# Performance work log

Measured on AMD Instinct MI355X. Metric: run time of the kernel, lower is better.

The kernel has to match this reference:

```python
import jax, jax.numpy as jnp
import numpy as np

N0 = N1 = 50000
E = 800000
IN = 128
OUT = 128
H = 8
DK = OUT // H  # 16
SQRT_DK = float(np.sqrt(DK))
T = 2  # node types


def setup_inputs() -> dict:
    key = jax.random.key(0)
    ks = jax.random.split(key, 24)
    s = 1.0 / np.sqrt(IN)
    inp = {
        "feat0": jax.random.normal(ks[0], (N0, IN), jnp.float32),
        "feat1": jax.random.normal(ks[1], (N1, IN), jnp.float32),
        "ev0": jax.random.uniform(ks[2], (E,), jnp.float32),
        "ev1": jax.random.uniform(ks[3], (E,), jnp.float32),
        "ev2": jax.random.uniform(ks[4], (E,), jnp.float32),
        "src0": jax.random.randint(ks[5], (E,), 0, N0),   # t0 -> t1
        "dst0": jax.random.randint(ks[6], (E,), 0, N1),
        "src1": jax.random.randint(ks[7], (E,), 0, N1),   # t1 -> t0
        "dst1": jax.random.randint(ks[8], (E,), 0, N0),
        "src2": jax.random.randint(ks[9], (E,), 0, N0),   # t0 -> t0
        "dst2": jax.random.randint(ks[10], (E,), 0, N0),
        # per-node-type parameters, stacked over T types
        "Kw": jax.random.normal(ks[11], (T, IN, OUT), jnp.float32) * s,
        "Kb": jnp.zeros((T, OUT), jnp.float32),
        "Qw": jax.random.normal(ks[12], (T, IN, OUT), jnp.float32) * s,
        "Qb": jnp.zeros((T, OUT), jnp.float32),
        "Vw": jax.random.normal(ks[13], (T, IN, OUT), jnp.float32) * s,
        "Vb": jnp.zeros((T, OUT), jnp.float32),
        "Aw": jax.random.normal(ks[14], (T, OUT, OUT), jnp.float32) * s,
        "Ab": jnp.zeros((T, OUT), jnp.float32),
        "ew": jax.random.normal(ks[15], (), jnp.float32),  # e_linear weight (1x1)
        "eb": jnp.zeros((), jnp.float32),                  # e_linear bias
        "skip": jnp.ones((T,), jnp.float32),
    }
    return inp


def _etype_agg(feat_s, feat_d, ts, td, src, dst, ev, n_dst,
               Kw, Kb, Qw, Qb, Vw, Vb, ew, eb):
    """One canonical etype: gather q.k per edge, edge_softmax over dst, u_mul_e + sum."""
    k = (feat_s @ Kw[ts] + Kb[ts]).reshape(-1, H, DK)
    v = (feat_s @ Vw[ts] + Vb[ts]).reshape(-1, H, DK)
    q = (feat_d @ Qw[td] + Qb[td]).reshape(-1, H, DK)
    # per-edge dot(q[dst], k[src]) over d_k -> [E, H]
    score = jnp.einsum('ehd,ehd->eh', q[dst], k[src])
    ea = ev[:, None] * ew + eb                     # e_linear on scalar edge feature, [E,1]
    score = score * ea / SQRT_DK                   # [E, H]
    # segmented softmax over incoming edges per destination node, per head
    m = jax.ops.segment_max(score, dst, num_segments=n_dst)
    ex = jnp.exp(score - m[dst])
    z = jax.ops.segment_sum(ex, dst, num_segments=n_dst)
    attn = ex / z[dst]                             # [E, H]
    msg = v[src] * attn[:, :, None]                # [E, H, DK]
    return jax.ops.segment_sum(msg, dst, num_segments=n_dst)  # [n_dst, H, DK]


def reference(feat0, feat1, ev0, ev1, ev2, src0, dst0, src1, dst1, src2, dst2,
              Kw, Kb, Qw, Qb, Vw, Vb, Aw, Ab, ew, eb, skip):
    # etype (t0,e0,t1)
    agg1 = _etype_agg(feat0, feat1, 0, 1, src0, dst0, ev0, N1,
                      Kw, Kb, Qw, Qb, Vw, Vb, ew, eb)
    # etypes targeting t0: (t1,e1,t0) and (t0,e2,t0); cross_reducer='mean'
    agg0a = _etype_agg(feat1, feat0, 1, 0, src1, dst1, ev1, N0,
                       Kw, Kb, Qw, Qb, Vw, Vb, ew, eb)
    agg0b = _etype_agg(feat0, feat0, 0, 0, src2, dst2, ev2, N0,
                       Kw, Kb, Qw, Qb, Vw, Vb, ew, eb)
    agg0 = 0.5 * (agg0a + agg0b)

    def _out(agg, feat, nid):
        t = agg.reshape(-1, OUT)
        trans = t @ Aw[nid] + Ab[nid]              # dropout omitted (eval mode)
        alpha = jax.nn.sigmoid(skip[nid])
        return trans * alpha + feat * (1.0 - alpha)

    h0 = _out(agg0, feat0, 0)
    h1 = _out(agg1, feat1, 1)
    return (h0, h1)
```

## Files before the change

kernel.cpp:

```cpp
#include <hip/hip_runtime.h>
#include <hip/hip_bf16.h>
#include <hip/hip_fp16.h>
#include <math.h>


#define NDIM 128
#define NRNG 32
#define NBK 512
#define UNITS (NBK * 4)
#define HSPAN 2048

typedef __attribute__((ext_vector_type(8))) short short8;
typedef __attribute__((ext_vector_type(4))) float f32x4;

__device__ __forceinline__ float bf2f(unsigned short u) {
    union { unsigned int i; float f; } x; x.i = ((unsigned int)u) << 16; return x.f;
}
__device__ __forceinline__ unsigned short f2bf(float f) {
    unsigned int u = __float_as_uint(f);
    unsigned int r = (u + 0x7FFFu + ((u >> 16) & 1u)) >> 16;
    return (unsigned short)r;
}
__device__ __forceinline__ int range_of(int d, int n) {
    return (int)(((long long)d * NRNG) / n);
}

__global__ void wt_prep(const float* __restrict__ Kw, const float* __restrict__ Qw,
                        const float* __restrict__ Vw, const float* __restrict__ Aw,
                        unsigned short* __restrict__ Wtbuf)
{
    const int b = blockIdx.x;
    const int t = b >> 2, m = b & 3;
    const float* src = (m == 0 ? Kw : m == 1 ? Qw : m == 2 ? Vw : Aw) + (size_t)t * 16384;
    unsigned short* dst = Wtbuf + (size_t)b * 16384;
    for (int i = threadIdx.x; i < 16384; i += blockDim.x) {
        const int k = i >> 7, nn = i & 127;
        dst[nn * 128 + k] = f2bf(src[i]);
    }
}

__global__ __launch_bounds__(256) void gemm_kqv(
    const float* __restrict__ feat0, const float* __restrict__ feat1,
    const unsigned short* __restrict__ Wtbuf,
    const float* __restrict__ Kb, const float* __restrict__ Qb, const float* __restrict__ Vb,
    unsigned short* __restrict__ K0o, unsigned short* __restrict__ Q0o, unsigned short* __restrict__ V0o,
    unsigned short* __restrict__ K1o, unsigned short* __restrict__ Q1o, unsigned short* __restrict__ V1o,
    int n0, int n1, int blocks0)
{
    const int b = blockIdx.x;
    const bool t1 = (b >= blocks0);
    const float* feat = t1 ? feat1 : feat0;
    const int n = t1 ? n1 : n0;
    const int boff = t1 ? NDIM : 0;
    const unsigned short* Wt = Wtbuf + (t1 ? 4 * 16384 : 0);
    unsigned short* outs[3];
    outs[0] = t1 ? K1o : K0o; outs[1] = t1 ? Q1o : Q0o; outs[2] = t1 ? V1o : V0o;
    const float* biases[3] = {Kb + boff, Qb + boff, Vb + boff};

    const int tid = threadIdx.x;
    const int w = tid >> 6, lane = tid & 63;
    const int r16 = lane & 15, kg = lane >> 4;
    const int brow = (t1 ? b - blocks0 : b) * 64;
    const int arow = min(brow + w * 16 + r16, n - 1);

    __shared__ float sacc[64][129];

    short8 afr[4];
#pragma unroll
    for (int k0i = 0; k0i < 4; ++k0i) {
        const float* ap = feat + (size_t)arow * NDIM + k0i * 32 + kg * 8;
        const float4 lo = *(const float4*)ap;
        const float4 hi = *(const float4*)(ap + 4);
        short8 a;
        a[0] = (short)f2bf(lo.x); a[1] = (short)f2bf(lo.y);
        a[2] = (short)f2bf(lo.z); a[3] = (short)f2bf(lo.w);
        a[4] = (short)f2bf(hi.x); a[5] = (short)f2bf(hi.y);
        a[6] = (short)f2bf(hi.z); a[7] = (short)f2bf(hi.w);
        afr[k0i] = a;
    }
    const int c8 = (lane & 15) * 8;
#pragma unroll
    for (int m = 0; m < 3; ++m) {
        const unsigned short* wt = Wt + (size_t)m * 16384;
        f32x4 acc[8];
#pragma unroll
        for (int c = 0; c < 8; ++c) acc[c] = (f32x4){0.f, 0.f, 0.f, 0.f};
#pragma unroll
        for (int k0i = 0; k0i < 4; ++k0i)
#pragma unroll
            for (int c = 0; c < 8; ++c) {
                const short8 bb = *(const short8*)(wt + (size_t)(16 * c + r16) * NDIM + k0i * 32 + kg * 8);
                acc[c] = __builtin_amdgcn_mfma_f32_16x16x32_bf16(afr[k0i], bb, acc[c], 0, 0, 0);
            }
        __syncthreads();
#pragma unroll
        for (int c = 0; c < 8; ++c)
#pragma unroll
            for (int j = 0; j < 4; ++j)
                sacc[w * 16 + kg * 4 + j][16 * c + r16] = acc[c][j];
        __syncthreads();
        const float4 blo = *(const float4*)(biases[m] + c8);
        const float4 bhi = *(const float4*)(biases[m] + c8 + 4);
        const float bias8[8] = {blo.x, blo.y, blo.z, blo.w, bhi.x, bhi.y, bhi.z, bhi.w};
#pragma unroll
        for (int j = 0; j < 4; ++j) {
            const int rloc = w * 16 + (lane >> 4) + j * 4;
            const int grow = brow + rloc;
            if (grow < n) {
                short8 o;
#pragma unroll
                for (int i = 0; i < 8; ++i)
                    o[i] = (short)f2bf(sacc[rloc][c8 + i] + bias8[i]);
                *(short8*)(outs[m] + (size_t)grow * NDIM + c8) = o;
            }
        }
    }
}

__global__ __launch_bounds__(256) void gemm_out(
    const unsigned short* __restrict__ aggb0a, const unsigned short* __restrict__ aggb0b,
    const unsigned short* __restrict__ aggb1,
    const unsigned short* __restrict__ Wtbuf, const float* __restrict__ Ab,
    const float* __restrict__ feat0, const float* __restrict__ feat1,
    const float* __restrict__ skip, float* __restrict__ out,
    int n0, int n1, int blocks0)
{
    const int b = blockIdx.x;
    const bool t1 = (b >= blocks0);
    const int n = t1 ? n1 : n0;
    const unsigned short* A1 = t1 ? aggb1 : aggb0a;
    const unsigned short* A2 = t1 ? (const unsigned short*)nullptr : aggb0b;
    const unsigned short* Wt = Wtbuf + (t1 ? 7 : 3) * 16384;
    const float* bias = Ab + (t1 ? NDIM : 0);
    const float* feat = t1 ? feat1 : feat0;
    float* C = out + (t1 ? (size_t)n0 * NDIM : 0);
    const int nid = t1 ? 1 : 0;

    const int tid = threadIdx.x;
    const int w = tid >> 6, lane = tid & 63;
    const int r16 = lane & 15, kg = lane >> 4;
    const int brow = (t1 ? b - blocks0 : b) * 64;
    const int arow = min(brow + w * 16 + r16, n - 1);

    __shared__ float sacc[64][129];

    short8 afr[4];
#pragma unroll
    for (int k0i = 0; k0i < 4; ++k0i) {
        short8 a = *(const short8*)(A1 + (size_t)arow * NDIM + k0i * 32 + kg * 8);
        if (!t1) {
            const short8 bb = *(const short8*)(A2 + (size_t)arow * NDIM + k0i * 32 + kg * 8);
#pragma unroll
            for (int j = 0; j < 8; ++j) {
                const float v = 0.5f * (bf2f((unsigned short)a[j]) + bf2f((unsigned short)bb[j]));
                a[j] = (short)f2bf(v);
            }
        }
        afr[k0i] = a;
    }
    f32x4 acc[8];
#pragma unroll
    for (int c = 0; c < 8; ++c) acc[c] = (f32x4){0.f, 0.f, 0.f, 0.f};
#pragma unroll
    for (int k0i = 0; k0i < 4; ++k0i)
#pragma unroll
        for (int c = 0; c < 8; ++c) {
            const short8 bb = *(const short8*)(Wt + (size_t)(16 * c + r16) * NDIM + k0i * 32 + kg * 8);
            acc[c] = __builtin_amdgcn_mfma_f32_16x16x32_bf16(afr[k0i], bb, acc[c], 0, 0, 0);
        }
    __syncthreads();
#pragma unroll
    for (int c = 0; c < 8; ++c)
#pragma unroll
        for (int j = 0; j < 4; ++j)
            sacc[w * 16 + kg * 4 + j][16 * c + r16] = acc[c][j];
    __syncthreads();

    const float sk = skip[nid];
    const float alpha = 1.f / (1.f + __expf(-sk));
    const float beta = 1.f - alpha;
    const int c8 = (lane & 15) * 8;
    const float4 blo = *(const float4*)(bias + c8);
    const float4 bhi = *(const float4*)(bias + c8 + 4);
#pragma unroll
    for (int j = 0; j < 4; ++j) {
        const int rloc = w * 16 + (lane >> 4) + j * 4;
        const int grow = brow + rloc;
        if (grow < n) {
            const float4 fa = *(const float4*)(feat + (size_t)grow * NDIM + c8);
            const float4 fb = *(const float4*)(feat + (size_t)grow * NDIM + c8 + 4);
            float4 oa, ob;
            oa.x = (sacc[rloc][c8 + 0] + blo.x) * alpha + fa.x * beta;
            oa.y = (sacc[rloc][c8 + 1] + blo.y) * alpha + fa.y * beta;
            oa.z = (sacc[rloc][c8 + 2] + blo.z) * alpha + fa.z * beta;
            oa.w = (sacc[rloc][c8 + 3] + blo.w) * alpha + fa.w * beta;
            ob.x = (sacc[rloc][c8 + 4] + bhi.x) * alpha + fb.x * beta;
            ob.y = (sacc[rloc][c8 + 5] + bhi.y) * alpha + fb.y * beta;
            ob.z = (sacc[rloc][c8 + 6] + bhi.z) * alpha + fb.z * beta;
            ob.w = (sacc[rloc][c8 + 7] + bhi.w) * alpha + fb.w * beta;
            *(float4*)(C + (size_t)grow * NDIM + c8) = oa;
            *(float4*)(C + (size_t)grow * NDIM + c8 + 4) = ob;
        }
    }
}

__global__ __launch_bounds__(256) void bucket_count(
    const int* __restrict__ d0, int E0, const int* __restrict__ d1, int E1,
    const int* __restrict__ d2, int E2, int n0, int n1, int* __restrict__ cnts)
{
    const int seg = blockIdx.y;
    const int* dst = seg == 0 ? d0 : (seg == 1 ? d1 : d2);
    const int E = seg == 0 ? E0 : (seg == 1 ? E1 : E2);
    const int ns = seg == 0 ? n1 : n0;
    const int unit = blockIdx.x * 4 + (threadIdx.x >> 6);
    const int lane = threadIdx.x & 63;
    const int span = (E + UNITS - 1) / UNITS;
    const int b = unit * span;
    const int e = min(b + span, E);

    int run[NRNG];
#pragma unroll
    for (int r0 = 0; r0 < NRNG; ++r0) run[r0] = 0;
    for (int i0 = b; i0 < e; i0 += 64) {
        const int i = i0 + lane;
        const bool v = i < e;
        const int d = v ? dst[i] : 0;
        const unsigned int r = v ? (unsigned int)range_of(d, ns) : 0xFFu;
#pragma unroll
        for (int r0 = 0; r0 < NRNG; ++r0)
            run[r0] += __popcll(__ballot(r == (unsigned int)r0));
    }
    if (lane == 0) {
        int* c = cnts + ((size_t)seg * UNITS + unit) * NRNG;
#pragma unroll
        for (int r0 = 0; r0 < NRNG; ++r0) c[r0] = run[r0];
    }
}

__global__ __launch_bounds__(256) void bucket_scan(int* __restrict__ cnts, int* __restrict__ rcur)
{
    const int seg = blockIdx.x >> 5;
    const int r = blockIdx.x & 31;
    const int t = threadIdx.x, lane = t & 63, w = t >> 6;

    int v[8];
    int run = 0;
#pragma unroll
    for (int j = 0; j < 8; ++j) {
        const int u = t * 8 + j;
        const int x = cnts[((size_t)seg * UNITS + u) * NRNG + r];
        v[j] = run;
        run += x;
    }
    const int tsum = run;
    int x = tsum;
#pragma unroll
    for (int o = 1; o < 64; o <<= 1) {
        const int y = __shfl_up(x, o);
        if (lane >= o) x += y;
    }
    const int wexc = x - tsum;
    __shared__ int wsum[4];
    if (lane == 63) wsum[w] = x;
    __syncthreads();
    int wbase = 0;
    for (int i = 0; i < w; ++i) wbase += wsum[i];
    const int base = wbase + wexc;
#pragma unroll
    for (int j = 0; j < 8; ++j) {
        const int u = t * 8 + j;
        cnts[((size_t)seg * UNITS + u) * NRNG + r] = base + v[j];
    }
    if (t == 255) rcur[seg * NRNG + r] = base + tsum;
}

__global__ __launch_bounds__(256) void bucket_write(
    const int* __restrict__ d0, const int* __restrict__ s0, const float* __restrict__ e0, int E0,
    const int* __restrict__ d1, const int* __restrict__ s1, const float* __restrict__ e1, int E1,
    const int* __restrict__ d2, const int* __restrict__ s2, const float* __restrict__ e2, int E2,
    int n0, int n1, const float* __restrict__ ew, const float* __restrict__ eb,
    const int* __restrict__ cnts, uint2* __restrict__ stg, int cap)
{
    const int seg = blockIdx.y;
    const int* dst = seg == 0 ? d0 : (seg == 1 ? d1 : d2);
    const int* src = seg == 0 ? s0 : (seg == 1 ? s1 : s2);
    const float* ev = seg == 0 ? e0 : (seg == 1 ? e1 : e2);
    const int E = seg == 0 ? E0 : (seg == 1 ? E1 : E2);
    const int ns = seg == 0 ? n1 : n0;
    const int unit = blockIdx.x * 4 + (threadIdx.x >> 6);
    const int lane = threadIdx.x & 63;
    const int span = (E + UNITS - 1) / UNITS;
    const int b = unit * span;
    const int e = min(b + span, E);
    const float LOG2E = 1.4426950408889634f;
    const float ews = ew[0] * 0.25f * LOG2E;
    const float ebs = eb[0] * 0.25f * LOG2E;
    uint2* sbase = stg + (size_t)seg * NRNG * cap;

    int run[NRNG];
    {
        const int* c = cnts + ((size_t)seg * UNITS + unit) * NRNG;
#pragma unroll
        for (int r0 = 0; r0 < NRNG; ++r0) run[r0] = c[r0];
    }
    for (int i0 = b; i0 < e; i0 += 64) {
        const int i = i0 + lane;
        const bool v = i < e;
        int d = 0, s = 0; float ee = 0.f;
        if (v) { d = dst[i]; s = src[i]; ee = ev[i]; }
        const unsigned int r = v ? (unsigned int)range_of(d, ns) : 0xFFu;
#pragma unroll
        for (int r0 = 0; r0 < NRNG; ++r0) {
            const unsigned long long m = __ballot(r == (unsigned int)r0);
            if (m == 0ull) continue;
            if (r == (unsigned int)r0) {
                const int off = run[r0] + __popcll(m & ((1ull << lane) - 1ull));
                sbase[(size_t)r0 * cap + off] =
                    make_uint2((unsigned int)d | ((unsigned int)s << 16), __float_as_uint(ee * ews + ebs));
            }
            run[r0] += __popcll(m);
        }
    }
}

__global__ __launch_bounds__(1024) void sortB(
    const uint2* __restrict__ stg, int cap, const int* __restrict__ rcur,
    int nA, int* __restrict__ offA, unsigned int* __restrict__ gA,
    int nB, int* __restrict__ offB, unsigned int* __restrict__ gB,
    int nC, int* __restrict__ offC, unsigned int* __restrict__ gC)
{
    const int seg = blockIdx.y;
    const int r = blockIdx.x;
    const int n = seg == 0 ? nA : (seg == 1 ? nB : nC);
    int* off = seg == 0 ? offA : (seg == 1 ? offB : offC);
    unsigned int* edg = seg == 0 ? gA : (seg == 1 ? gB : gC);
    const int cnt = rcur[seg * NRNG + r];
    const uint2* s = stg + ((size_t)seg * NRNG + r) * cap;
    const int dbase = (int)(((long long)r * n + NRNG - 1) / NRNG);
    const int dnext = (int)(((long long)(r + 1) * n + NRNG - 1) / NRNG);
    const int span = dnext - dbase;
    int ebase = 0;
    for (int i = 0; i < r; ++i) ebase += rcur[seg * NRNG + i];

    __shared__ int hist[HSPAN];
    __shared__ int wsum[16];
    const int tid = threadIdx.x, lane = tid & 63, wid = tid >> 6;

    for (int i = tid; i < span; i += 1024) hist[i] = 0;
    __syncthreads();
    for (int i = tid; i < cnt; i += 1024)
        atomicAdd(&hist[(int)(s[i].x & 0xFFFFu) - dbase], 1);
    __syncthreads();
    const int C = (span + 1023) >> 10;
    int v[4];
    int run = 0;
    const int b0 = tid * C;
#pragma unroll 4
    for (int j = 0; j < C; ++j) {
        const int i = b0 + j;
        const int x = (i < span) ? hist[i] : 0;
        v[j] = run;
        run += x;
    }
    int x = run;
#pragma unroll
    for (int o = 1; o < 64; o <<= 1) {
        const int y = __shfl_up(x, o);
        if (lane >= o) x += y;
    }
    if (lane == 63) wsum[wid] = x;
    __syncthreads();
    int wbase = 0;
    for (int i = 0; i < wid; ++i) wbase += wsum[i];
    const int tb = ebase + wbase + (x - run);
#pragma unroll 4
    for (int j = 0; j < C; ++j) {
        const int i = b0 + j;
        if (i < span) hist[i] = tb + v[j];
    }
    __syncthreads();
    for (int i = tid; i < span; i += 1024) off[dbase + i] = hist[i];
    if (r == NRNG - 1 && tid == 0) off[n] = ebase + cnt;
    __syncthreads();
    for (int i = tid; i < cnt; i += 1024) {
        const uint2 e = s[i];
        const int d = (int)(e.x & 0xFFFFu);
        const int p = atomicAdd(&hist[d - dbase], 1);
        const float wf = __uint_as_float(e.y);
        const __half hh = __float2half(wf);
        edg[p] = (e.x >> 16) | ((unsigned int)__half_as_ushort(hh) << 16);
    }
}

__global__ __launch_bounds__(256) void edge_agg3(
    const int* __restrict__ off0, const unsigned int* __restrict__ edg0,
    const unsigned short* __restrict__ K0e, const unsigned short* __restrict__ Q0e,
    const unsigned short* __restrict__ V0e, unsigned short* __restrict__ out0, int nd0,
    const int* __restrict__ off1, const unsigned int* __restrict__ edg1,
    const unsigned short* __restrict__ K1e, const unsigned short* __restrict__ Q1e,
    const unsigned short* __restrict__ V1e, unsigned short* __restrict__ out1, int nd1,
    const int* __restrict__ off2, const unsigned int* __restrict__ edg2,
    const unsigned short* __restrict__ K2e, const unsigned short* __restrict__ Q2e,
    const unsigned short* __restrict__ V2e, unsigned short* __restrict__ out2, int nd2)
{
    const int seg = blockIdx.y;
    const int* off = seg == 0 ? off0 : (seg == 1 ? off1 : off2);
    const unsigned int* edg = seg == 0 ? edg0 : (seg == 1 ? edg1 : edg2);
    const unsigned short* K = seg == 0 ? K0e : (seg == 1 ? K1e : K2e);
    const unsigned short* Q = seg == 0 ? Q0e : (seg == 1 ? Q1e : Q2e);
    const unsigned short* V = seg == 0 ? V0e : (seg == 1 ? V1e : V2e);
    unsigned short* aggb = seg == 0 ? out0 : (seg == 1 ? out1 : out2);
    const int n_dst = seg == 0 ? nd0 : (seg == 1 ? nd1 : nd2);

    const int wv = (blockIdx.x * blockDim.x + threadIdx.x) >> 6;
    const int lane = threadIdx.x & 63;
    const int half = lane >> 5, l5 = lane & 31;
    const int dst = 2 * wv + half;
    const bool valid = dst < n_dst;
    int beg = 0, len = 0;
    if (valid) { beg = off[dst]; len = off[dst + 1] - beg; }
    const int maxLen = max(len, __shfl_xor(len, 32));
    if (maxLen == 0) {
        if (valid) *(ushort4*)(aggb + (size_t)dst * NDIM + 4 * l5) = (ushort4){0, 0, 0, 0};
        return;
    }
    float qx = 0.f, qy = 0.f, qz = 0.f, qw = 0.f;
    if (valid) {
        const ushort4 qr = *(const ushort4*)(Q + (size_t)dst * NDIM + 4 * l5);
        qx = bf2f(qr.x); qy = bf2f(qr.y); qz = bf2f(qr.z); qw = bf2f(qr.w);
    }
    float zA = 0.f, aA0 = 0.f, aA1 = 0.f, aA2 = 0.f, aA3 = 0.f;
    float zB = 0.f, aB0 = 0.f, aB1 = 0.f, aB2 = 0.f, aB3 = 0.f;

    unsigned int ec = (l5 < len) ? edg[beg + l5] : 0u;
    for (int t0 = 0; t0 < maxLen; t0 += 32) {
        unsigned int en = 0u;
        const int t0n = t0 + 32;
        if (t0n < maxLen && t0n + l5 < len) en = edg[beg + t0n + l5];
        const int lim = min(32, maxLen - t0);
        for (int u = 0; u < lim; u += 2) {
            const int sl0 = (half << 5) + u;
            const unsigned int v0 = (unsigned int)__shfl((int)ec, sl0);
            const unsigned int v1 = (unsigned int)__shfl((int)ec, sl0 + 1);
            const bool act0 = (t0 + u) < len;
            const bool act1 = (u + 1 < lim) && ((t0 + u + 1) < len);
            const int s0 = (int)(v0 & 0xFFFFu);
            const int s1 = (int)(v1 & 0xFFFFu);
            const float w0 = __half2float(__ushort_as_half((unsigned short)(v0 >> 16)));
            const float w1 = __half2float(__ushort_as_half((unsigned short)(v1 >> 16)));
            const ushort4 kr0 = *(const ushort4*)(K + (size_t)s0 * NDIM + 4 * l5);
            const ushort4 vr0 = *(const ushort4*)(V + (size_t)s0 * NDIM + 4 * l5);
            const ushort4 kr1 = *(const ushort4*)(K + (size_t)s1 * NDIM + 4 * l5);
            const ushort4 vr1 = *(const ushort4*)(V + (size_t)s1 * NDIM + 4 * l5);
            float d0 = qx * bf2f(kr0.x) + qy * bf2f(kr0.y) + qz * bf2f(kr0.z) + qw * bf2f(kr0.w);
            float d1 = qx * bf2f(kr1.x) + qy * bf2f(kr1.y) + qz * bf2f(kr1.z) + qw * bf2f(kr1.w);
            d0 += __shfl_xor(d0, 1);
            d1 += __shfl_xor(d1, 1);
            d0 += __shfl_xor(d0, 2);
            d1 += __shfl_xor(d1, 2);
            const float p0 = act0 ? exp2f(d0 * w0) : 0.f;
            const float p1 = act1 ? exp2f(d1 * w1) : 0.f;
            zA += p0;
            aA0 += p0 * bf2f(vr0.x); aA1 += p0 * bf2f(vr0.y);
            aA2 += p0 * bf2f(vr0.z); aA3 += p0 * bf2f(vr0.w);
            zB += p1;
            aB0 += p1 * bf2f(vr1.x); aB1 += p1 * bf2f(vr1.y);
            aB2 += p1 * bf2f(vr1.z); aB3 += p1 * bf2f(vr1.w);
        }
        ec = en;
    }
    if (valid) {
        const float z = zA + zB;
        const float inv = (len > 0) ? 1.f / z : 0.f;
        ushort4 o;
        o.x = f2bf((aA0 + aB0) * inv); o.y = f2bf((aA1 + aB1) * inv);
        o.z = f2bf((aA2 + aB2) * inv); o.w = f2bf((aA3 + aB3) * inv);
        *(ushort4*)(aggb + (size_t)dst * NDIM + 4 * l5) = o;
    }
}

extern "C" void kernel_launch(void* const* d_in, const int* in_sizes, int n_in,
                              void* d_out, int out_size, void* d_ws, size_t ws_size,
                              hipStream_t stream)
{
    const float* feat0 = (const float*)d_in[0];
    const float* feat1 = (const float*)d_in[1];
    const float* ev0 = (const float*)d_in[2];
    const float* ev1 = (const float*)d_in[3];
    const float* ev2 = (const float*)d_in[4];
    const int* src0 = (const int*)d_in[5];
    const int* dst0 = (const int*)d_in[6];
    const int* src1 = (const int*)d_in[7];
    const int* dst1 = (const int*)d_in[8];
    const int* src2 = (const int*)d_in[9];
    const int* dst2 = (const int*)d_in[10];
    const float* Kw = (const float*)d_in[11];
    const float* Kb = (const float*)d_in[12];
    const float* Qw = (const float*)d_in[13];
    const float* Qb = (const float*)d_in[14];
    const float* Vw = (const float*)d_in[15];
    const float* Vb = (const float*)d_in[16];
    const float* Aw = (const float*)d_in[17];
    const float* Ab = (const float*)d_in[18];
    const float* ew = (const float*)d_in[19];
    const float* eb = (const float*)d_in[20];
    const float* skip = (const float*)d_in[21];

    const int n0 = in_sizes[0] / NDIM;
    const int n1 = in_sizes[1] / NDIM;
    const int E0 = in_sizes[5];
    const int E1 = in_sizes[7];
    const int E2 = in_sizes[9];
    if (max(n0, n1) > 65504) return;
    const int Emax = max(E0, max(E1, E2));
    const int cap = Emax / NRNG + 8192;

    auto rup = [](size_t b) { return (b + 255) & ~size_t(255); };
    const size_t need =
        rup((size_t)8 * 16384 * 2) +
        rup((size_t)n0 * NDIM * 2) * 3 +
        rup((size_t)n1 * NDIM * 2) * 3 +
        rup((size_t)n1 * NDIM * 2) +
        rup((size_t)n0 * NDIM * 2) * 2 +
        rup((size_t)(n1 + 1) * 4) +
        rup((size_t)(n0 + 1) * 4) * 2 +
        rup((size_t)128 * 4) +
        rup((size_t)3 * UNITS * NRNG * 4) +
        rup((size_t)3 * NRNG * cap * 8) +
        rup((size_t)E0 * 4) + rup((size_t)E1 * 4) + rup((size_t)E2 * 4);
    if (ws_size < need) return;

    char* p = (char*)d_ws;
    auto alloc = [&](size_t bytes) -> char* {
        char* r = p;
        p += (bytes + 255) & ~size_t(255);
        return r;
    };
    unsigned short* Wtbuf = (unsigned short*)alloc((size_t)8 * 16384 * 2);
    unsigned short* K0 = (unsigned short*)alloc((size_t)n0 * NDIM * 2);
    unsigned short* Q0 = (unsigned short*)alloc((size_t)n0 * NDIM * 2);
    unsigned short* V0 = (unsigned short*)alloc((size_t)n0 * NDIM * 2);
    unsigned short* K1 = (unsigned short*)alloc((size_t)n1 * NDIM * 2);
    unsigned short* Q1 = (unsigned short*)alloc((size_t)n1 * NDIM * 2);
    unsigned short* V1 = (unsigned short*)alloc((size_t)n1 * NDIM * 2);
    unsigned short* aggb1  = (unsigned short*)alloc((size_t)n1 * NDIM * 2);
    unsigned short* aggb0a = (unsigned short*)alloc((size_t)n0 * NDIM * 2);
    unsigned short* aggb0b = (unsigned short*)alloc((size_t)n0 * NDIM * 2);
    int* off0 = (int*)alloc((size_t)(n1 + 1) * 4);
    int* off1 = (int*)alloc((size_t)(n0 + 1) * 4);
    int* off2 = (int*)alloc((size_t)(n0 + 1) * 4);
    int* rcur = (int*)alloc((size_t)128 * 4);
    int* cnts = (int*)alloc((size_t)3 * UNITS * NRNG * 4);
    uint2* stg = (uint2*)alloc((size_t)3 * NRNG * cap * 8);
    unsigned int* edg0 = (unsigned int*)alloc((size_t)E0 * 4);
    unsigned int* edg1 = (unsigned int*)alloc((size_t)E1 * 4);
    unsigned int* edg2 = (unsigned int*)alloc((size_t)E2 * 4);

    dim3 blk(256);
    const int blocks0 = (n0 + 63) / 64, blocks1 = (n1 + 63) / 64;

    wt_prep<<<8, 256, 0, stream>>>(Kw, Qw, Vw, Aw, Wtbuf);
    gemm_kqv<<<blocks0 + blocks1, blk, 0, stream>>>(feat0, feat1, Wtbuf, Kb, Qb, Vb,
                                                    K0, Q0, V0, K1, Q1, V1, n0, n1, blocks0);

    bucket_count<<<dim3(NBK, 3), blk, 0, stream>>>(dst0, E0, dst1, E1, dst2, E2, n0, n1, cnts);
    bucket_scan<<<3 * NRNG, blk, 0, stream>>>(cnts, rcur);
    bucket_write<<<dim3(NBK, 3), blk, 0, stream>>>(dst0, src0, ev0, E0,
                                                   dst1, src1, ev1, E1,
                                                   dst2, src2, ev2, E2,
                                                   n0, n1, ew, eb, cnts, stg, cap);
    sortB<<<dim3(NRNG, 3), 1024, 0, stream>>>(stg, cap, rcur,
                                              n1, off0, edg0,
                                              n0, off1, edg1,
                                              n0, off2, edg2);

    const int nmax = (n0 > n1) ? n0 : n1;
    const int ebx = ((nmax + 1) / 2 + 3) / 4;
    edge_agg3<<<dim3(ebx, 3), blk, 0, stream>>>(
        off0, edg0, K0, Q1, V0, aggb1, n1,
        off1, edg1, K1, Q0, V1, aggb0a, n0,
        off2, edg2, K0, Q0, V0, aggb0b, n0);

    gemm_out<<<blocks0 + blocks1, blk, 0, stream>>>(aggb0a, aggb0b, aggb1, Wtbuf, Ab,
                                                    feat0, feat1, skip, (float*)d_out,
                                                    n0, n1, blocks0);
}
```

Measured before the change: 419.3 us.

## Store K/Q as fp16 and use fdot2 for edge scores; tile weight transpose

K and Q projections are now written as fp16 instead of bf16, which lets the edge attention kernel compute the q·k partial dot product with packed fp16 dot2 instructions instead of unpacking and multiplying four scalars. The weight prep kernel is rewritten to transpose through shared memory with vectorized loads and stores. This cuts ALU work in the edge loop and makes the small prep kernel more efficient. In exchange, fp16 has a narrower exponent range than bf16, so large K/Q values could overflow.

```diff
diff --git a/kernel.cpp b/kernel.cpp
--- a/kernel.cpp
+++ b/kernel.cpp
@@ -12,6 +12,7 @@
 
 typedef __attribute__((ext_vector_type(8))) short short8;
 typedef __attribute__((ext_vector_type(4))) float f32x4;
+typedef __attribute__((ext_vector_type(2))) _Float16 half2v;
 
 __device__ __forceinline__ float bf2f(unsigned short u) {
     union { unsigned int i; float f; } x; x.i = ((unsigned int)u) << 16; return x.f;
@@ -24,18 +25,38 @@
 __device__ __forceinline__ int range_of(int d, int n) {
     return (int)(((long long)d * NRNG) / n);
 }
-
-__global__ void wt_prep(const float* __restrict__ Kw, const float* __restrict__ Qw,
-                        const float* __restrict__ Vw, const float* __restrict__ Aw,
-                        unsigned short* __restrict__ Wtbuf)
+union U4h { ushort4 u; struct { half2v a, b; } h; };
+
+__global__ __launch_bounds__(256) void wt_prep(const float* __restrict__ Kw, const float* __restrict__ Qw,
+                                               const float* __restrict__ Vw, const float* __restrict__ Aw,
+                                               unsigned short* __restrict__ Wtbuf)
 {
     const int b = blockIdx.x;
     const int t = b >> 2, m = b & 3;
     const float* src = (m == 0 ? Kw : m == 1 ? Qw : m == 2 ? Vw : Aw) + (size_t)t * 16384;
     unsigned short* dst = Wtbuf + (size_t)b * 16384;
-    for (int i = threadIdx.x; i < 16384; i += blockDim.x) {
-        const int k = i >> 7, nn = i & 127;
-        dst[nn * 128 + k] = f2bf(src[i]);
+    const int tid = threadIdx.x;
+    __shared__ float tile[64][132];
+#pragma unroll
+    for (int h = 0; h < 2; ++h) {
+        const int k0 = h * 64;
+        for (int idx = tid; idx < 64 * 32; idx += 256) {
+            const int kr = idx >> 5;
+            const int c4 = (idx & 31) * 4;
+            const float4 v = *(const float4*)(src + (size_t)(k0 + kr) * 128 + c4);
+            tile[kr][c4 + 0] = v.x; tile[kr][c4 + 1] = v.y;
+            tile[kr][c4 + 2] = v.z; tile[kr][c4 + 3] = v.w;
+        }
+        __syncthreads();
+        for (int idx = tid; idx < 128 * 16; idx += 256) {
+            const int nn = idx >> 4;
+            const int kk4 = (idx & 15) * 4;
+            ushort4 o;
+            o.x = f2bf(tile[kk4 + 0][nn]); o.y = f2bf(tile[kk4 + 1][nn]);
+            o.z = f2bf(tile[kk4 + 2][nn]); o.w = f2bf(tile[kk4 + 3][nn]);
+            *(ushort4*)(dst + (size_t)nn * 128 + k0 + kk4) = o;
+        }
+        __syncthreads();
     }
 }
 
@@ -109,8 +130,11 @@
             if (grow < n) {
                 short8 o;
 #pragma unroll
-                for (int i = 0; i < 8; ++i)
-                    o[i] = (short)f2bf(sacc[rloc][c8 + i] + bias8[i]);
+                for (int i = 0; i < 8; ++i) {
+                    const float x = sacc[rloc][c8 + i] + bias8[i];
+                    o[i] = (m < 2) ? (short)__half_as_ushort(__float2half(x))
+                                   : (short)f2bf(x);
+                }
                 *(short8*)(outs[m] + (size_t)grow * NDIM + c8) = o;
             }
         }
@@ -424,11 +448,11 @@
         if (valid) *(ushort4*)(aggb + (size_t)dst * NDIM + 4 * l5) = (ushort4){0, 0, 0, 0};
         return;
     }
-    float qx = 0.f, qy = 0.f, qz = 0.f, qw = 0.f;
-    if (valid) {
-        const ushort4 qr = *(const ushort4*)(Q + (size_t)dst * NDIM + 4 * l5);
-        qx = bf2f(qr.x); qy = bf2f(qr.y); qz = bf2f(qr.z); qw = bf2f(qr.w);
-    }
+    U4h q;
+    q.u = make_ushort4(0, 0, 0, 0);
+    if (valid) q.u = *(const ushort4*)(Q + (size_t)dst * NDIM + 4 * l5);
+    const half2v q01 = q.h.a, q23 = q.h.b;
+
     float zA = 0.f, aA0 = 0.f, aA1 = 0.f, aA2 = 0.f, aA3 = 0.f;
     float zB = 0.f, aB0 = 0.f, aB1 = 0.f, aB2 = 0.f, aB3 = 0.f;
 
@@ -448,12 +472,22 @@
             const int s1 = (int)(v1 & 0xFFFFu);
             const float w0 = __half2float(__ushort_as_half((unsigned short)(v0 >> 16)));
             const float w1 = __half2float(__ushort_as_half((unsigned short)(v1 >> 16)));
-            const ushort4 kr0 = *(const ushort4*)(K + (size_t)s0 * NDIM + 4 * l5);
+            U4h k0u, k1u;
+            k0u.u = *(const ushort4*)(K + (size_t)s0 * NDIM + 4 * l5);
+            k1u.u = *(const ushort4*)(K + (size_t)s1 * NDIM + 4 * l5);
             const ushort4 vr0 = *(const ushort4*)(V + (size_t)s0 * NDIM + 4 * l5);
-            const ushort4 kr1 = *(const ushort4*)(K + (size_t)s1 * NDIM + 4 * l5);
             const ushort4 vr1 = *(const ushort4*)(V + (size_t)s1 * NDIM + 4 * l5);
-            float d0 = qx * bf2f(kr0.x) + qy * bf2f(kr0.y) + qz * bf2f(kr0.z) + qw * bf2f(kr0.w);
-            float d1 = qx * bf2f(kr1.x) + qy * bf2f(kr1.y) + qz * bf2f(kr1.z) + qw * bf2f(kr1.w);
+#if __has_builtin(__builtin_amdgcn_fdot2)
+            float d0 = __builtin_amdgcn_fdot2(k0u.h.a, q01, 0.f, false);
+            d0 = __builtin_amdgcn_fdot2(k0u.h.b, q23, d0, false);
+            float d1 = __builtin_amdgcn_fdot2(k1u.h.a, q01, 0.f, false);
+            d1 = __builtin_amdgcn_fdot2(k1u.h.b, q23, d1, false);
+#else
+            float d0 = (float)k0u.h.a[0] * (float)q01[0] + (float)k0u.h.a[1] * (float)q01[1]
+                     + (float)k0u.h.b[0] * (float)q23[0] + (float)k0u.h.b[1] * (float)q23[1];
+            float d1 = (float)k1u.h.a[0] * (float)q01[0] + (float)k1u.h.a[1] * (float)q01[1]
+                     + (float)k1u.h.b[0] * (float)q23[0] + (float)k1u.h.b[1] * (float)q23[1];
+#endif
             d0 += __shfl_xor(d0, 1);
             d1 += __shfl_xor(d1, 1);
             d0 += __shfl_xor(d0, 2);
```

After: 396.0 us, median of 3. 1.06x faster.
